# Optimization experiments

Hardware: AMD Instinct MI355X
Metric: run time of the kernel (lower is better)

## Reference

```python
import jax, jax.numpy as jnp
import numpy as np

B, N, T, D = 256, 64, 60, 128
H = 128  # gate hidden dims


def setup_inputs() -> dict:
    key = jax.random.key(0)
    ks = jax.random.split(key, 5)
    x = jax.random.normal(ks[0], (B, N, T, D), dtype=jnp.float32)
    s = 1.0 / np.sqrt(D)
    sg_w1 = jax.random.normal(ks[1], (D, H), dtype=jnp.float32) * s
    sg_b1 = jnp.zeros((H,), dtype=jnp.float32)
    sg_w2 = jax.random.normal(ks[2], (H, 1), dtype=jnp.float32) * (1.0 / np.sqrt(H))
    sg_b2 = jnp.zeros((1,), dtype=jnp.float32)
    tg_w1 = jax.random.normal(ks[3], (D, H), dtype=jnp.float32) * s
    tg_b1 = jnp.zeros((H,), dtype=jnp.float32)
    tg_w2 = jax.random.normal(ks[4], (H, 1), dtype=jnp.float32) * (1.0 / np.sqrt(H))
    tg_b2 = jnp.zeros((1,), dtype=jnp.float32)
    return {"x": x, "sg_w1": sg_w1, "sg_b1": sg_b1, "sg_w2": sg_w2, "sg_b2": sg_b2,
            "tg_w1": tg_w1, "tg_b1": tg_b1, "tg_w2": tg_w2, "tg_b2": tg_b2}


def reference(x, sg_w1, sg_b1, sg_w2, sg_b2, tg_w1, tg_b1, tg_w2, tg_b2):
    # Spatial attentional aggregation, vectorized over all timesteps at once.
    # Segment softmax over batch_index == softmax over the node axis (regular segments).
    gate = jnp.tanh(x @ sg_w1 + sg_b1) @ sg_w2 + sg_b2          # [B, N, T, 1]
    alpha = jax.nn.softmax(gate, axis=1)                        # softmax over nodes
    pooled = jnp.sum(alpha * x, axis=1)                         # [B, T, D]
    # Temporal attention pooling over the sequence axis.
    score = jnp.tanh(pooled @ tg_w1 + tg_b1) @ tg_w2 + tg_b2    # [B, T, 1]
    tw = jax.nn.softmax(score, axis=1)                          # [B, T, 1]
    final = jnp.sum(tw * pooled, axis=1)                        # [B, D]
    return final, tw
```

## Files before the change

### kernel.cpp

```cpp
#include <hip/hip_runtime.h>

#define B_ 256
#define N_ 64
#define T_ 60
#define D_ 128
#define H_ 128

typedef __attribute__((ext_vector_type(8))) short short8;
typedef __attribute__((ext_vector_type(4))) float f32x4;

__device__ __forceinline__ unsigned short f2bf(float f) {
  unsigned int u = __builtin_bit_cast(unsigned int, f);
  u = u + 0x7FFFu + ((u >> 16) & 1u);
  return (unsigned short)(u >> 16);
}

__device__ __forceinline__ float tanh_fast(float x) {
  float e = __builtin_amdgcn_exp2f(x * 2.885390081777927f);
  return 1.0f - 2.0f * __builtin_amdgcn_rcpf(e + 1.0f);
}

#define GLOAD_LDS16(gp, lp)                                        \
  __builtin_amdgcn_global_load_lds(                                \
      (const __attribute__((address_space(1))) void*)(gp),         \
      (__attribute__((address_space(3))) void*)(lp), 16, 0, 0)

__global__ __launch_bounds__(256) void prep_weights(
    const float* __restrict__ sg_w1, const float* __restrict__ tg_w1,
    unsigned short* __restrict__ wfrag) {
  int tid = blockIdx.x * 256 + threadIdx.x;
  if (tid >= 2 * 4 * 8 * 64) return;
  int l  = tid & 63;
  int nt = (tid >> 6) & 7;
  int kt = (tid >> 9) & 3;
  int m  = tid >> 11;
  const float* W = m ? tg_w1 : sg_w1;
  int n  = nt * 16 + (l & 15);
  int k0 = kt * 32 + 8 * (l >> 4);
  unsigned short* dst = wfrag + (size_t)tid * 8;
#pragma unroll
  for (int i = 0; i < 8; ++i) dst[i] = f2bf(W[(k0 + i) * H_ + n]);
}

__global__ __launch_bounds__(256, 4) void spatial_kernel(
    const float* __restrict__ x,
    const short8* __restrict__ wfrag,
    const float* __restrict__ b1,
    const float* __restrict__ w2,
    float* __restrict__ pooled) {
  __shared__ __align__(16) float xs[64 * 128];
  __shared__ float gpart[2][64];
  __shared__ float pp[2][128];

  const int tid = threadIdx.x;
  const int bid = blockIdx.x;
  const int b = bid / T_;
  const int t = bid - b * T_;

  const char* xbc = (const char*)(x + (size_t)b * (N_ * T_ * D_) + (size_t)t * D_);

#pragma unroll
  for (int it = 0; it < 8; ++it) {
    int q = it * 256 + tid;
    int n = q >> 5;
    unsigned soff = (unsigned)n * (T_ * D_ * 4) + ((((q & 31) * 16)) ^ ((n & 7) << 4));
    GLOAD_LDS16(xbc + soff, (char*)xs + it * 4096 + (tid & 192) * 16);
  }
  __syncthreads();

  const int l  = tid & 63;
  const int w  = tid >> 6;
  const int lg = l >> 4;
  const int lr = l & 15;
  const int wr = w >> 1;
  const int wc = w & 1;

  float b1v[4], w2v[4];
#pragma unroll
  for (int ntl = 0; ntl < 4; ++ntl) {
    b1v[ntl] = b1[wc * 64 + ntl * 16 + lr];
    w2v[ntl] = w2[wc * 64 + ntl * 16 + lr];
  }

  f32x4 acc[2][4];
#pragma unroll
  for (int mt = 0; mt < 2; ++mt)
#pragma unroll
    for (int ntl = 0; ntl < 4; ++ntl) acc[mt][ntl] = (f32x4)(0.0f);

#pragma unroll
  for (int kt = 0; kt < 4; ++kt) {
#pragma unroll
    for (int mt = 0; mt < 2; ++mt) {
      const int row = 32 * wr + 16 * mt + lr;
      const int byte0 = row * 512 + (((kt * 8 + 2 * lg) * 16) ^ ((row & 7) << 4));
      f32x4 a0 = *(const f32x4*)((const char*)xs + byte0);
      f32x4 a1 = *(const f32x4*)((const char*)xs + (byte0 ^ 16));
      short8 af;
      af[0] = (short)f2bf(a0[0]); af[1] = (short)f2bf(a0[1]);
      af[2] = (short)f2bf(a0[2]); af[3] = (short)f2bf(a0[3]);
      af[4] = (short)f2bf(a1[0]); af[5] = (short)f2bf(a1[1]);
      af[6] = (short)f2bf(a1[2]); af[7] = (short)f2bf(a1[3]);
#pragma unroll
      for (int ntl = 0; ntl < 4; ++ntl) {
        short8 bf = wfrag[(kt * 8 + wc * 4 + ntl) * 64 + l];
        acc[mt][ntl] = __builtin_amdgcn_mfma_f32_16x16x32_bf16(af, bf, acc[mt][ntl], 0, 0, 0);
      }
    }
  }

#pragma unroll
  for (int mt = 0; mt < 2; ++mt) {
#pragma unroll
    for (int j = 0; j < 4; ++j) {
      float s = 0.f;
#pragma unroll
      for (int ntl = 0; ntl < 4; ++ntl) {
        float h = acc[mt][ntl][j] + b1v[ntl];
        s += tanh_fast(h) * w2v[ntl];
      }
      s += __shfl_xor(s, 1);
      s += __shfl_xor(s, 2);
      s += __shfl_xor(s, 4);
      s += __shfl_xor(s, 8);
      if (lr == 0) gpart[wc][32 * wr + 16 * mt + 4 * lg + j] = s;
    }
  }
  __syncthreads();

  float g = gpart[0][l] + gpart[1][l];
  float p = __builtin_amdgcn_exp2f(g * 1.4426950408889634f);
  float sm = p;
  sm += __shfl_xor(sm, 32);
  sm += __shfl_xor(sm, 16);
  sm += __shfl_xor(sm, 8);
  sm += __shfl_xor(sm, 4);
  sm += __shfl_xor(sm, 2);
  sm += __shfl_xor(sm, 1);
  const float alpha = p * __builtin_amdgcn_rcpf(sm);

  {
    const int c  = tid & 127;
    const int hh = tid >> 7;
    const unsigned cbase = 4u * c;
    float s = 0.f;
#pragma unroll
    for (int i = 0; i < 32; ++i) {
      const int n = 32 * hh + i;
      const float av = __shfl(alpha, n);
      const float xv = *(const float*)((const char*)xs + ((cbase ^ ((unsigned)(n & 7) << 4)) + (unsigned)n * 512));
      s += av * xv;
    }
    pp[hh][c] = s;
  }
  __syncthreads();

  if (tid < 128)
    pooled[((size_t)b * T_ + t) * D_ + tid] = pp[0][tid] + pp[1][tid];
}

__global__ __launch_bounds__(256) void temporal_kernel(
    const float* __restrict__ pooled,
    const short8* __restrict__ wfrag,
    const float* __restrict__ b1,
    const float* __restrict__ w2,
    float* __restrict__ out) {
  __shared__ float xs[64][132];
  __shared__ float score_lds[64];
  __shared__ float tw_lds[64];
  __shared__ float pp[2][128];

  const int tid = threadIdx.x;
  const int b = blockIdx.x;

  const float* pb = pooled + (size_t)b * T_ * D_;
#pragma unroll
  for (int it = 0; it < 8; ++it) {
    int q = it * 256 + tid;
    int n = q >> 5;
    int c4 = (q & 31) << 2;
    float4 v = {0.f, 0.f, 0.f, 0.f};
    if (n < T_) v = *(const float4*)(pb + n * D_ + c4);
    *(float4*)(&xs[n][c4]) = v;
  }
  __syncthreads();

  const int l = tid & 63;
  const int w = tid >> 6;
  const int lg = l >> 4;
  const int lr = l & 15;

  float b1v[8], w2v[8];
#pragma unroll
  for (int nt = 0; nt < 8; ++nt) {
    b1v[nt] = b1[nt * 16 + lr];
    w2v[nt] = w2[nt * 16 + lr];
  }

  f32x4 acc[8];
#pragma unroll
  for (int nt = 0; nt < 8; ++nt) acc[nt] = (f32x4)(0.0f);

  const int row = 16 * w + lr;
#pragma unroll
  for (int kt = 0; kt < 4; ++kt) {
    const int k0 = kt * 32 + 8 * lg;
    float4 a0 = *(const float4*)(&xs[row][k0]);
    float4 a1 = *(const float4*)(&xs[row][k0 + 4]);
    short8 af;
    af[0] = (short)f2bf(a0.x); af[1] = (short)f2bf(a0.y);
    af[2] = (short)f2bf(a0.z); af[3] = (short)f2bf(a0.w);
    af[4] = (short)f2bf(a1.x); af[5] = (short)f2bf(a1.y);
    af[6] = (short)f2bf(a1.z); af[7] = (short)f2bf(a1.w);
#pragma unroll
    for (int nt = 0; nt < 8; ++nt) {
      short8 bf = wfrag[(kt * 8 + nt) * 64 + l];
      acc[nt] = __builtin_amdgcn_mfma_f32_16x16x32_bf16(af, bf, acc[nt], 0, 0, 0);
    }
  }

#pragma unroll
  for (int j = 0; j < 4; ++j) {
    float s = 0.f;
#pragma unroll
    for (int nt = 0; nt < 8; ++nt) {
      float h = acc[nt][j] + b1v[nt];
      s += tanh_fast(h) * w2v[nt];
    }
    s += __shfl_xor(s, 1);
    s += __shfl_xor(s, 2);
    s += __shfl_xor(s, 4);
    s += __shfl_xor(s, 8);
    if (lr == 0) score_lds[16 * w + 4 * lg + j] = s;
  }
  __syncthreads();

  float p = (l < T_) ? __builtin_amdgcn_exp2f(score_lds[l] * 1.4426950408889634f) : 0.f;
  float sm = p;
  sm += __shfl_xor(sm, 32);
  sm += __shfl_xor(sm, 16);
  sm += __shfl_xor(sm, 8);
  sm += __shfl_xor(sm, 4);
  sm += __shfl_xor(sm, 2);
  sm += __shfl_xor(sm, 1);
  float tw = p / sm;
  if (w == 0) {
    tw_lds[l] = tw;
    if (l < T_) out[B_ * D_ + b * T_ + l] = tw;
  }
  __syncthreads();

  const int c = tid & 127;
  const int hh = tid >> 7;
  float s = 0.f;
#pragma unroll
  for (int i = 0; i < 30; ++i) {
    int tt = 30 * hh + i;
    s += tw_lds[tt] * xs[tt][c];
  }
  pp[hh][c] = s;
  __syncthreads();
  if (tid < 128) out[(size_t)b * D_ + tid] = pp[0][tid] + pp[1][tid];
}

extern "C" void kernel_launch(void* const* d_in, const int* in_sizes, int n_in,
                              void* d_out, int out_size, void* d_ws, size_t ws_size,
                              hipStream_t stream) {
  const float* x     = (const float*)d_in[0];
  const float* sg_w1 = (const float*)d_in[1];
  const float* sg_b1 = (const float*)d_in[2];
  const float* sg_w2 = (const float*)d_in[3];
  const float* tg_w1 = (const float*)d_in[5];
  const float* tg_b1 = (const float*)d_in[6];
  const float* tg_w2 = (const float*)d_in[7];
  float* out = (float*)d_out;

  unsigned short* wfrag = (unsigned short*)d_ws;
  float* pooled = (float*)((char*)d_ws + 65536);

  prep_weights<<<16, 256, 0, stream>>>(sg_w1, tg_w1, wfrag);
  spatial_kernel<<<B_ * T_, 256, 0, stream>>>(
      x, (const short8*)wfrag, sg_b1, sg_w2, pooled);
  temporal_kernel<<<B_, 256, 0, stream>>>(
      pooled, (const short8*)(wfrag + 16384), tg_b1, tg_w2, out);
}
```

Baseline: 157.1 us.

## Load x into registers, store bf16 tile in LDS, pool from registers

Replaces the async global-to-LDS fp32 staging of the 64x128 x tile with register loads, converted once to bf16 and stored into a padded LDS tile. MFMA A-fragments are then read directly as short8 with no per-use conversion. The weighted pooling now uses the x values still held in registers plus shuffle reductions, which removes the LDS reread, the partial-sum buffer and a barrier. This halves LDS footprint, which may raise occupancy, but it gives up the direct-to-LDS async load and adds register pressure from holding 8 float4 per thread.

```diff
diff --git a/kernel.cpp b/kernel.cpp
--- a/kernel.cpp
+++ b/kernel.cpp
@@ -19,11 +19,6 @@
   float e = __builtin_amdgcn_exp2f(x * 2.885390081777927f);
   return 1.0f - 2.0f * __builtin_amdgcn_rcpf(e + 1.0f);
 }
-
-#define GLOAD_LDS16(gp, lp)                                        \
-  __builtin_amdgcn_global_load_lds(                                \
-      (const __attribute__((address_space(1))) void*)(gp),         \
-      (__attribute__((address_space(3))) void*)(lp), 16, 0, 0)
 
 __global__ __launch_bounds__(256) void prep_weights(
     const float* __restrict__ sg_w1, const float* __restrict__ tg_w1,
@@ -48,23 +43,31 @@
     const float* __restrict__ b1,
     const float* __restrict__ w2,
     float* __restrict__ pooled) {
-  __shared__ __align__(16) float xs[64 * 128];
+  __shared__ __align__(16) char xs16[64 * 272];
   __shared__ float gpart[2][64];
-  __shared__ float pp[2][128];
 
   const int tid = threadIdx.x;
   const int bid = blockIdx.x;
   const int b = bid / T_;
   const int t = bid - b * T_;
 
-  const char* xbc = (const char*)(x + (size_t)b * (N_ * T_ * D_) + (size_t)t * D_);
-
-#pragma unroll
-  for (int it = 0; it < 8; ++it) {
-    int q = it * 256 + tid;
-    int n = q >> 5;
-    unsigned soff = (unsigned)n * (T_ * D_ * 4) + ((((q & 31) * 16)) ^ ((n & 7) << 4));
-    GLOAD_LDS16(xbc + soff, (char*)xs + it * 4096 + (tid & 192) * 16);
+  const float* xb = x + (size_t)b * (N_ * T_ * D_) + (size_t)t * D_;
+
+  const int cg  = tid >> 3;
+  const int sub = tid & 7;
+
+  float4 px[8];
+#pragma unroll
+  for (int r = 0; r < 8; ++r) {
+    const int n = sub + 8 * r;
+    px[r] = *(const float4*)(xb + (size_t)n * (T_ * D_) + 4 * cg);
+  }
+#pragma unroll
+  for (int r = 0; r < 8; ++r) {
+    const int n = sub + 8 * r;
+    unsigned lo = ((unsigned)f2bf(px[r].y) << 16) | f2bf(px[r].x);
+    unsigned hi = ((unsigned)f2bf(px[r].w) << 16) | f2bf(px[r].z);
+    *(uint2*)(xs16 + n * 272 + cg * 8) = make_uint2(lo, hi);
   }
   __syncthreads();
 
@@ -93,14 +96,7 @@
 #pragma unroll
     for (int mt = 0; mt < 2; ++mt) {
       const int row = 32 * wr + 16 * mt + lr;
-      const int byte0 = row * 512 + (((kt * 8 + 2 * lg) * 16) ^ ((row & 7) << 4));
-      f32x4 a0 = *(const f32x4*)((const char*)xs + byte0);
-      f32x4 a1 = *(const f32x4*)((const char*)xs + (byte0 ^ 16));
-      short8 af;
-      af[0] = (short)f2bf(a0[0]); af[1] = (short)f2bf(a0[1]);
-      af[2] = (short)f2bf(a0[2]); af[3] = (short)f2bf(a0[3]);
-      af[4] = (short)f2bf(a1[0]); af[5] = (short)f2bf(a1[1]);
-      af[6] = (short)f2bf(a1[2]); af[7] = (short)f2bf(a1[3]);
+      short8 af = *(const short8*)(xs16 + row * 272 + kt * 64 + lg * 16);
 #pragma unroll
       for (int ntl = 0; ntl < 4; ++ntl) {
         short8 bf = wfrag[(kt * 8 + wc * 4 + ntl) * 64 + l];
@@ -139,24 +135,25 @@
   sm += __shfl_xor(sm, 1);
   const float alpha = p * __builtin_amdgcn_rcpf(sm);
 
-  {
-    const int c  = tid & 127;
-    const int hh = tid >> 7;
-    const unsigned cbase = 4u * c;
-    float s = 0.f;
-#pragma unroll
-    for (int i = 0; i < 32; ++i) {
-      const int n = 32 * hh + i;
-      const float av = __shfl(alpha, n);
-      const float xv = *(const float*)((const char*)xs + ((cbase ^ ((unsigned)(n & 7) << 4)) + (unsigned)n * 512));
-      s += av * xv;
-    }
-    pp[hh][c] = s;
-  }
-  __syncthreads();
-
-  if (tid < 128)
-    pooled[((size_t)b * T_ + t) * D_ + tid] = pp[0][tid] + pp[1][tid];
+  f32x4 q = (f32x4)(0.0f);
+#pragma unroll
+  for (int r = 0; r < 8; ++r) {
+    const int n = sub + 8 * r;
+    const float av = __shfl(alpha, n);
+    q[0] += av * px[r].x;
+    q[1] += av * px[r].y;
+    q[2] += av * px[r].z;
+    q[3] += av * px[r].w;
+  }
+#pragma unroll
+  for (int m = 1; m <= 4; m <<= 1) {
+    q[0] += __shfl_xor(q[0], m);
+    q[1] += __shfl_xor(q[1], m);
+    q[2] += __shfl_xor(q[2], m);
+    q[3] += __shfl_xor(q[3], m);
+  }
+  if (sub == 0)
+    *(f32x4*)(pooled + ((size_t)b * T_ + t) * D_ + 4 * cg) = q;
 }
 
 __global__ __launch_bounds__(256) void temporal_kernel(
```

Result: no change. 154.1 us (-1.9%).
